# Kernel optimization log

Hardware: AMD Instinct MI355X
Metric: run time of the kernel (lower is better)

## Reference

```python
import jax, jax.numpy as jnp
import numpy as np

B, N, D = 2, 512, 256
H, HD = 4, 64  # hidden_dim=256 split across 4 heads (is_concat=True)
SLOPE = 0.2


def setup_inputs() -> dict:
    key = jax.random.key(0)
    ks = jax.random.split(key, 8)
    rn = lambda k, sh: jax.random.normal(k, sh, dtype=jnp.float32)
    return {
        "query": rn(ks[0], (B, N, D)),
        "key_in": rn(ks[1], (B, N, D)),
        "value": rn(ks[2], (B, N, D)),
        "w_q": rn(ks[3], (D, H * HD)) * 0.05,  # shared query/key projection (share_weights=True)
        "b_q": rn(ks[4], (H * HD,)) * 0.05,
        "w_v": rn(ks[5], (D, H * HD)) * 0.05,
        "b_v": rn(ks[6], (H * HD,)) * 0.05,
        "a": rn(ks[7], (HD,)) * 0.05,  # attention Linear(hd, 1, bias=False), shared across heads
    }


def reference(query, key_in, value, w_q, b_q, w_v, b_v, a):
    hq = (query @ w_q + b_q).reshape(B, N, H, HD)
    hk = (key_in @ w_q + b_q).reshape(B, N, H, HD)  # share_weights=True
    hv = (value @ w_v + b_v).reshape(B, N, H, HD)
    # torch repeat/repeat_interleave + view gives h[b,i,j] = hq[b,j] + hk[b,i]
    h = hq[:, None, :, :, :] + hk[:, :, None, :, :]  # [B, N, N, H, HD]
    e = jnp.einsum('bijhf,f->bijh', jax.nn.leaky_relu(h, SLOPE), a)
    e = jax.nn.softmax(e, axis=2)  # softmax over source nodes j (dropout is identity in eval)
    out = jnp.einsum('bijh,bjhf->bihf', e, hv).reshape(B, N, H * HD)  # is_concat
    h_prime = jax.nn.relu(out)
    return h_prime, e
```

## Files before the change

kernel.cpp:

```cpp
#include <hip/hip_runtime.h>


#define NB 2
#define NN 512
#define DD 256
#define NH 4
#define HDIM 64

__device__ __forceinline__ float rl(float v, int u) {
    return __uint_as_float(__builtin_amdgcn_readlane(__float_as_uint(v), u));
}

__global__ __launch_bounds__(256, 4) void proj_kernel(
    const float* __restrict__ q, const float* __restrict__ kin, const float* __restrict__ vin,
    const float* __restrict__ wq, const float* __restrict__ bq,
    const float* __restrict__ wv, const float* __restrict__ bv,
    float* __restrict__ hq, float* __restrict__ hk, float* __restrict__ hv)
{
    const int m = blockIdx.z;
    const float* x    = (m == 0) ? q  : (m == 1) ? kin : vin;
    const float* w    = (m == 2) ? wv : wq;
    const float* bias = (m == 2) ? bv : bq;
    float* out        = (m == 0) ? hq : (m == 1) ? hk : hv;

    const int r0 = blockIdx.x * 16;
    const int cb = blockIdx.y * 128;
    const int t  = threadIdx.x;

    __shared__ float xs[16][DD + 4];

    #pragma unroll
    for (int p = 0; p < 4; ++p) {
        const int idx = t + 256 * p;
        const int row = idx >> 6;
        const int kc  = idx & 63;
        const float4 v = *reinterpret_cast<const float4*>(&x[(size_t)(r0 + row) * DD + kc * 4]);
        *reinterpret_cast<float4*>(&xs[row][kc * 4]) = v;
    }
    __syncthreads();

    const int row0 = (t >> 5) * 2;
    const int c0   = (t & 31) * 4;

    const float4 b4 = *reinterpret_cast<const float4*>(&bias[cb + c0]);
    float acc[2][4];
    #pragma unroll
    for (int r = 0; r < 2; ++r) { acc[r][0]=b4.x; acc[r][1]=b4.y; acc[r][2]=b4.z; acc[r][3]=b4.w; }

    for (int kt = 0; kt < DD; kt += 4) {
        const float4 a0 = *reinterpret_cast<const float4*>(&xs[row0][kt]);
        const float4 a1 = *reinterpret_cast<const float4*>(&xs[row0 + 1][kt]);
        const float xa0[4] = {a0.x, a0.y, a0.z, a0.w};
        const float xa1[4] = {a1.x, a1.y, a1.z, a1.w};
        #pragma unroll
        for (int kk = 0; kk < 4; ++kk) {
            const float4 w4 = *reinterpret_cast<const float4*>(&w[(size_t)(kt + kk) * DD + cb + c0]);
            const float wv4[4] = {w4.x, w4.y, w4.z, w4.w};
            #pragma unroll
            for (int c = 0; c < 4; ++c) {
                acc[0][c] = fmaf(xa0[kk], wv4[c], acc[0][c]);
                acc[1][c] = fmaf(xa1[kk], wv4[c], acc[1][c]);
            }
        }
    }
    #pragma unroll
    for (int r = 0; r < 2; ++r) {
        float4 o; o.x = acc[r][0]; o.y = acc[r][1]; o.z = acc[r][2]; o.w = acc[r][3];
        *reinterpret_cast<float4*>(&out[(size_t)(r0 + row0 + r) * DD + cb + c0]) = o;
    }
}

__global__ __launch_bounds__(512, 4) void attn_kernel(
    const float* __restrict__ hq, const float* __restrict__ hk, const float* __restrict__ hv,
    const float* __restrict__ a, float* __restrict__ out_hp, float* __restrict__ out_e)
{
    const int t   = threadIdx.x;
    const int b   = blockIdx.x >> 8;
    const int rem = blockIdx.x & 255;
    const int i0  = (rem >> 1) * 4;
    const int hp  = rem & 1;

    __shared__ float skp[4][2][HDIM + 4];
    __shared__ float sa[HDIM];
    __shared__ float s[8][NN + 8];
    __shared__ float part[4][4][128];

    {
        const int ii = t >> 7, c = t & 127;
        skp[ii][c >> 6][c & 63] = hk[((size_t)(b * NN) + i0 + ii) * DD + hp * 128 + c];
    }
    if (t < HDIM) sa[t] = a[t];
    __syncthreads();

    {
        const int hl = t & 1;
        const int j0 = (t >> 1) * 2;
        const float* qbase = hq + ((size_t)(b * NN) + j0) * DD + (hp * 2 + hl) * HDIM;
        float accu[2] = {0.f, 0.f};
        float acc[2][4] = {};
        #pragma unroll
        for (int half = 0; half < 2; ++half) {
            float4 qb[16];
            #pragma unroll
            for (int fc = 0; fc < 8; ++fc) {
                qb[fc]     = *reinterpret_cast<const float4*>(qbase + half * 32 + fc * 4);
                qb[fc + 8] = *reinterpret_cast<const float4*>(qbase + DD + half * 32 + fc * 4);
            }
            #pragma unroll
            for (int fc = 0; fc < 8; ++fc) {
                const int fo = half * 32 + fc * 4;
                const float4 a4 = *reinterpret_cast<const float4*>(&sa[fo]);
                const float av[4] = {a4.x, a4.y, a4.z, a4.w};
                float kk[4][4];
                #pragma unroll
                for (int ii = 0; ii < 4; ++ii) {
                    const float4 kv = *reinterpret_cast<const float4*>(&skp[ii][hl][fo]);
                    kk[ii][0]=kv.x; kk[ii][1]=kv.y; kk[ii][2]=kv.z; kk[ii][3]=kv.w;
                }
                #pragma unroll
                for (int jj = 0; jj < 2; ++jj) {
                    const float4 q4 = qb[jj * 8 + fc];
                    const float qv[4] = {q4.x, q4.y, q4.z, q4.w};
                    #pragma unroll
                    for (int c = 0; c < 4; ++c) {
                        accu[jj] = fmaf(qv[c], av[c], accu[jj]);
                        #pragma unroll
                        for (int ii = 0; ii < 4; ++ii)
                            acc[jj][ii] = fmaf(__builtin_fabsf(qv[c] + kk[ii][c]), av[c], acc[jj][ii]);
                    }
                }
            }
        }
        #pragma unroll
        for (int jj = 0; jj < 2; ++jj) {
            const float su = 0.6f * accu[jj];
            #pragma unroll
            for (int ii = 0; ii < 4; ++ii)
                s[ii * 2 + hl][j0 + jj] = fmaf(0.4f, acc[jj][ii], su);
        }
    }
    __syncthreads();

    {
        const int wv = t >> 6, lane = t & 63;
        float* row = &s[wv][0];
        float vals[8]; float mx = -1e30f;
        #pragma unroll
        for (int k2 = 0; k2 < 8; ++k2) { vals[k2] = row[lane + 64 * k2]; mx = fmaxf(mx, vals[k2]); }
        #pragma unroll
        for (int off = 32; off; off >>= 1) mx = fmaxf(mx, __shfl_xor(mx, off, 64));
        float sum = 0.f;
        #pragma unroll
        for (int k2 = 0; k2 < 8; ++k2) { vals[k2] = __expf(vals[k2] - mx); sum += vals[k2]; }
        #pragma unroll
        for (int off = 32; off; off >>= 1) sum += __shfl_xor(sum, off, 64);
        const float inv = 1.0f / sum;
        #pragma unroll
        for (int k2 = 0; k2 < 8; ++k2) row[lane + 64 * k2] = vals[k2] * inv;
    }
    __syncthreads();

    {
        float* oe = out_e + ((size_t)(b * NN) + i0) * NN * NH + hp * 2;
        #pragma unroll
        for (int k2 = 0; k2 < 4; ++k2) {
            const int fi = t + 512 * k2;
            const int ii = fi >> 9;
            const int j  = fi & 511;
            float2 o; o.x = s[ii * 2 + 0][j]; o.y = s[ii * 2 + 1][j];
            *reinterpret_cast<float2*>(oe + (size_t)ii * NN * NH + j * NH) = o;
        }
    }

    {
        const int col  = t & 127;
        const int jg   = t >> 7;
        const int hl   = col >> 6;
        const int lane = t & 63;
        float acc[4] = {0.f, 0.f, 0.f, 0.f};
        const float* hvb = hv + (size_t)(b * NN) * DD + hp * 128 + col;
        #pragma unroll
        for (int ch = 0; ch < 2; ++ch) {
            const int jbase = jg * 128 + ch * 64;
            const float e0 = s[0 * 2 + hl][jbase + lane];
            const float e1 = s[1 * 2 + hl][jbase + lane];
            const float e2 = s[2 * 2 + hl][jbase + lane];
            const float e3 = s[3 * 2 + hl][jbase + lane];
            #pragma unroll
            for (int ub = 0; ub < 4; ++ub) {
                float hvv[16];
                #pragma unroll
                for (int k = 0; k < 16; ++k)
                    hvv[k] = hvb[(size_t)(jbase + ub * 16 + k) * DD];
                #pragma unroll
                for (int k = 0; k < 16; ++k) {
                    const int u = ub * 16 + k;
                    acc[0] = fmaf(rl(e0, u), hvv[k], acc[0]);
                    acc[1] = fmaf(rl(e1, u), hvv[k], acc[1]);
                    acc[2] = fmaf(rl(e2, u), hvv[k], acc[2]);
                    acc[3] = fmaf(rl(e3, u), hvv[k], acc[3]);
                }
            }
        }
        #pragma unroll
        for (int ii = 0; ii < 4; ++ii) part[jg][ii][col] = acc[ii];
    }
    __syncthreads();
    {
        const int ii = t >> 7, col = t & 127;
        const float v = part[0][ii][col] + part[1][ii][col] + part[2][ii][col] + part[3][ii][col];
        out_hp[((size_t)(b * NN) + i0 + ii) * DD + hp * 128 + col] = v > 0.f ? v : 0.f;
    }
}

extern "C" void kernel_launch(void* const* d_in, const int* in_sizes, int n_in,
                              void* d_out, int out_size, void* d_ws, size_t ws_size,
                              hipStream_t stream) {
    const float* q   = (const float*)d_in[0];
    const float* kin = (const float*)d_in[1];
    const float* vin = (const float*)d_in[2];
    const float* wq  = (const float*)d_in[3];
    const float* bq  = (const float*)d_in[4];
    const float* wv  = (const float*)d_in[5];
    const float* bv  = (const float*)d_in[6];
    const float* a   = (const float*)d_in[7];

    float* out_hp = (float*)d_out;
    float* out_e  = out_hp + (size_t)NB * NN * DD;

    float* hq = (float*)d_ws;
    float* hk = hq + (size_t)NB * NN * DD;
    float* hv = hk + (size_t)NB * NN * DD;

    proj_kernel<<<dim3(64, 2, 3), 256, 0, stream>>>(q, kin, vin, wq, bq, wv, bv, hq, hk, hv);
    attn_kernel<<<dim3(NB * 128 * 2), 512, 0, stream>>>(hq, hk, hv, a, out_hp, out_e);
}
```

Baseline: 131.2 us.

## Split attention blocks per head and read hk/a directly from global memory

The attention kernel now launches one 256-thread block per (batch, 4-row group, head) instead of one 512-thread block covering a head pair, which doubles the grid. The shared-memory staging of hk rows and the attention vector is removed: they are loaded straight from global memory as uniform addresses, which drops one barrier and shrinks shared memory. Scheduling barriers are added after the global load batches to keep loads grouped ahead of the math. The e writes become scalar stores with stride 4 floats rather than float2 stores, so store coalescing gets worse.

```diff
diff --git a/kernel.cpp b/kernel.cpp
--- a/kernel.cpp
+++ b/kernel.cpp
@@ -70,32 +70,24 @@
     }
 }
 
-__global__ __launch_bounds__(512, 4) void attn_kernel(
+__global__ __launch_bounds__(256, 4) void attn_kernel(
     const float* __restrict__ hq, const float* __restrict__ hk, const float* __restrict__ hv,
     const float* __restrict__ a, float* __restrict__ out_hp, float* __restrict__ out_e)
 {
     const int t   = threadIdx.x;
-    const int b   = blockIdx.x >> 8;
-    const int rem = blockIdx.x & 255;
-    const int i0  = (rem >> 1) * 4;
-    const int hp  = rem & 1;
-
-    __shared__ float skp[4][2][HDIM + 4];
-    __shared__ float sa[HDIM];
-    __shared__ float s[8][NN + 8];
-    __shared__ float part[4][4][128];
-
-    {
-        const int ii = t >> 7, c = t & 127;
-        skp[ii][c >> 6][c & 63] = hk[((size_t)(b * NN) + i0 + ii) * DD + hp * 128 + c];
-    }
-    if (t < HDIM) sa[t] = a[t];
-    __syncthreads();
-
-    {
-        const int hl = t & 1;
-        const int j0 = (t >> 1) * 2;
-        const float* qbase = hq + ((size_t)(b * NN) + j0) * DD + (hp * 2 + hl) * HDIM;
+    const int b   = blockIdx.x >> 9;
+    const int rem = blockIdx.x & 511;
+    const int i0  = (rem >> 2) * 4;
+    const int h   = rem & 3;
+
+    __shared__ float s[4][NN + 8];
+    __shared__ float part[4][4][HDIM];
+
+    const float* hk0 = hk + ((size_t)(b * NN) + i0) * DD + h * HDIM;
+
+    {
+        const int j0 = t * 2;
+        const float* qbase = hq + ((size_t)(b * NN) + j0) * DD + h * HDIM;
         float accu[2] = {0.f, 0.f};
         float acc[2][4] = {};
         #pragma unroll
@@ -106,15 +98,16 @@
                 qb[fc]     = *reinterpret_cast<const float4*>(qbase + half * 32 + fc * 4);
                 qb[fc + 8] = *reinterpret_cast<const float4*>(qbase + DD + half * 32 + fc * 4);
             }
+            __builtin_amdgcn_sched_barrier(0);
             #pragma unroll
             for (int fc = 0; fc < 8; ++fc) {
                 const int fo = half * 32 + fc * 4;
-                const float4 a4 = *reinterpret_cast<const float4*>(&sa[fo]);
+                const float4 a4 = *reinterpret_cast<const float4*>(a + fo);
                 const float av[4] = {a4.x, a4.y, a4.z, a4.w};
                 float kk[4][4];
                 #pragma unroll
                 for (int ii = 0; ii < 4; ++ii) {
-                    const float4 kv = *reinterpret_cast<const float4*>(&skp[ii][hl][fo]);
+                    const float4 kv = *reinterpret_cast<const float4*>(hk0 + ii * DD + fo);
                     kk[ii][0]=kv.x; kk[ii][1]=kv.y; kk[ii][2]=kv.z; kk[ii][3]=kv.w;
                 }
                 #pragma unroll
@@ -136,7 +129,7 @@
             const float su = 0.6f * accu[jj];
             #pragma unroll
             for (int ii = 0; ii < 4; ++ii)
-                s[ii * 2 + hl][j0 + jj] = fmaf(0.4f, acc[jj][ii], su);
+                s[ii][j0 + jj] = fmaf(0.4f, acc[jj][ii], su);
         }
     }
     __syncthreads();
@@ -161,55 +154,54 @@
     __syncthreads();
 
     {
-        float* oe = out_e + ((size_t)(b * NN) + i0) * NN * NH + hp * 2;
-        #pragma unroll
-        for (int k2 = 0; k2 < 4; ++k2) {
-            const int fi = t + 512 * k2;
-            const int ii = fi >> 9;
-            const int j  = fi & 511;
-            float2 o; o.x = s[ii * 2 + 0][j]; o.y = s[ii * 2 + 1][j];
-            *reinterpret_cast<float2*>(oe + (size_t)ii * NN * NH + j * NH) = o;
-        }
-    }
-
-    {
-        const int col  = t & 127;
-        const int jg   = t >> 7;
-        const int hl   = col >> 6;
+        float* oe = out_e + (((size_t)(b * NN) + i0) * NN) * NH + h;
+        #pragma unroll
+        for (int k2 = 0; k2 < 8; ++k2) {
+            const int idx = t + 256 * k2;
+            const int ii = idx >> 9;
+            const int j  = idx & 511;
+            oe[((size_t)ii * NN + j) * NH] = s[ii][j];
+        }
+    }
+
+    {
+        const int col  = t & 63;
+        const int jg   = t >> 6;
         const int lane = t & 63;
-        float acc[4] = {0.f, 0.f, 0.f, 0.f};
-        const float* hvb = hv + (size_t)(b * NN) * DD + hp * 128 + col;
+        float acc4[4] = {0.f, 0.f, 0.f, 0.f};
+        const float* hvb = hv + (size_t)(b * NN) * DD + h * HDIM + col;
         #pragma unroll
         for (int ch = 0; ch < 2; ++ch) {
             const int jbase = jg * 128 + ch * 64;
-            const float e0 = s[0 * 2 + hl][jbase + lane];
-            const float e1 = s[1 * 2 + hl][jbase + lane];
-            const float e2 = s[2 * 2 + hl][jbase + lane];
-            const float e3 = s[3 * 2 + hl][jbase + lane];
+            const float e0 = s[0][jbase + lane];
+            const float e1 = s[1][jbase + lane];
+            const float e2 = s[2][jbase + lane];
+            const float e3 = s[3][jbase + lane];
             #pragma unroll
             for (int ub = 0; ub < 4; ++ub) {
                 float hvv[16];
                 #pragma unroll
                 for (int k = 0; k < 16; ++k)
                     hvv[k] = hvb[(size_t)(jbase + ub * 16 + k) * DD];
+                __builtin_amdgcn_sched_barrier(0);
                 #pragma unroll
                 for (int k = 0; k < 16; ++k) {
                     const int u = ub * 16 + k;
-                    acc[0] = fmaf(rl(e0, u), hvv[k], acc[0]);
-                    acc[1] = fmaf(rl(e1, u), hvv[k], acc[1]);
-                    acc[2] = fmaf(rl(e2, u), hvv[k], acc[2]);
-                    acc[3] = fmaf(rl(e3, u), hvv[k], acc[3]);
+                    acc4[0] = fmaf(rl(e0, u), hvv[k], acc4[0]);
+                    acc4[1] = fmaf(rl(e1, u), hvv[k], acc4[1]);
+                    acc4[2] = fmaf(rl(e2, u), hvv[k], acc4[2]);
+                    acc4[3] = fmaf(rl(e3, u), hvv[k], acc4[3]);
                 }
             }
         }
         #pragma unroll
-        for (int ii = 0; ii < 4; ++ii) part[jg][ii][col] = acc[ii];
-    }
-    __syncthreads();
-    {
-        const int ii = t >> 7, col = t & 127;
+        for (int ii = 0; ii < 4; ++ii) part[jg][ii][col] = acc4[ii];
+    }
+    __syncthreads();
+    {
+        const int ii = t >> 6, col = t & 63;
         const float v = part[0][ii][col] + part[1][ii][col] + part[2][ii][col] + part[3][ii][col];
-        out_hp[((size_t)(b * NN) + i0 + ii) * DD + hp * 128 + col] = v > 0.f ? v : 0.f;
+        out_hp[((size_t)(b * NN) + i0 + ii) * DD + h * HDIM + col] = v > 0.f ? v : 0.f;
     }
 }
 
@@ -233,5 +225,5 @@
     float* hv = hk + (size_t)NB * NN * DD;
 
     proj_kernel<<<dim3(64, 2, 3), 256, 0, stream>>>(q, kin, vin, wq, bq, wv, bv, hq, hk, hv);
-    attn_kernel<<<dim3(NB * 128 * 2), 512, 0, stream>>>(hq, hk, hv, a, out_hp, out_e);
-}
+    attn_kernel<<<dim3(NB * 128 * NH), 256, 0, stream>>>(hq, hk, hv, a, out_hp, out_e);
+}
```

New measurement: 122.6 us. 1.07x faster.
